# Optimization experiments

Hardware: AMD Instinct MI355X
Metric: run time of the kernel (lower is better)

Reference implementation:

```python
import jax, jax.numpy as jnp
import numpy as np

K = 4096
D = 128
B = 8
T = 3000
EMA_DECAY = 0.99
EMA_EPS = 1e-05
DEAD_THRESHOLD = 2.0


def setup_inputs() -> dict:
    key = jax.random.key(0)
    k1, k2, k3 = jax.random.split(key, 3)
    z = jax.random.normal(k1, (B, D, T), dtype=jnp.float32)
    codebook = jax.random.normal(k2, (K, D), dtype=jnp.float32) * 0.05  # pretrained-like
    ema_cluster_size = jnp.ones((K,), dtype=jnp.float32)
    ema_embed_avg = codebook.copy()
    return {"z": z, "codebook": codebook,
            "ema_cluster_size": ema_cluster_size, "ema_embed_avg": ema_embed_avg}


def reference(z, codebook, ema_cluster_size, ema_embed_avg):
    b, d, t = z.shape
    z_t = jnp.transpose(z, (0, 2, 1))            # [B, T, D]
    z_flat = z_t.reshape(-1, d)                  # [N, D]

    x2 = jnp.sum(z_flat * z_flat, axis=1, keepdims=True)
    y2 = jnp.sum(codebook * codebook, axis=1)[None, :]
    distances = x2 + y2 - 2.0 * (z_flat @ codebook.T)
    indices = jnp.argmin(distances, axis=1)      # [N]

    q = codebook[indices].reshape(b, t, d)       # [B, T, D]
    loss_commit = jnp.mean((z_t - jax.lax.stop_gradient(q)) ** 2)

    # --- EMA update (torch: @torch.no_grad, training mode) ---
    zf = jax.lax.stop_gradient(z_flat)
    counts = jax.ops.segment_sum(jnp.ones_like(indices, dtype=jnp.float32), indices, num_segments=K)
    embed_sum = jax.ops.segment_sum(zf, indices, num_segments=K)   # [K, D]
    new_cs = ema_cluster_size * EMA_DECAY + counts * (1.0 - EMA_DECAY)
    new_ea = ema_embed_avg * EMA_DECAY + embed_sum * (1.0 - EMA_DECAY)
    n = jnp.sum(new_cs)
    cluster_size = (new_cs + EMA_EPS) / (n + K * EMA_EPS) * n
    embed = new_ea / jnp.clip(cluster_size, 1e-12)[:, None]

    # dead-code reset: resample dead entries from the batch
    dead = new_cs < DEAD_THRESHOLD                                 # [K] bool
    rand_idx = jax.random.randint(jax.random.key(42), (K,), 0, zf.shape[0])
    sampled = zf[rand_idx]                                          # [K, D]
    new_codebook = jnp.where(dead[:, None], sampled, embed)
    new_cs = jnp.where(dead, 1.0, new_cs)
    new_ea = jnp.where(dead[:, None], sampled, new_ea)

    # straight-through estimator
    q_ste = z_t + jax.lax.stop_gradient(q - z_t)
    z_q = jnp.transpose(q_ste, (0, 2, 1))        # [B, D, T]
    codes = indices.reshape(b, t)[None, :, None, :]  # [1, B, 1, T]

    return (z_q, codes, loss_commit, new_codebook, new_cs, new_ea)
```

## Files before the change

kernel.cpp:

```cpp
#include <hip/hip_runtime.h>
#include <stdint.h>

#define KCB 4096
#define DIM 128
#define BSZ 8
#define TLEN 3000
#define NPT 24000
#define KD (KCB*DIM)
#define BDT (BSZ*DIM*TLEN)

#define OFF_ZQ    0
#define OFF_CODES 3072000
#define OFF_LOSS  3096000
#define OFF_CB    3096001
#define OFF_CS    3620289
#define OFF_EA    3624385

#define OUT_ZH    0
#define OUT_ZL    1536000
#define OUT_CBH   3096004
#define OUT_CBL   3358148

#define WS_LOSS   0
#define WS_NTOT   1
#define WS_RCNT   2
#define WS_COUNTS 16
#define WS_Y2     (WS_COUNTS + 4096)
#define WS_X2     (WS_Y2 + 4096)
#define WS_CS0    (WS_X2 + 24000)
#define WS_RAND   (WS_CS0 + 4096)
#define WS_IDX    (WS_RAND + 4096)
#define WS_RLIST  (WS_IDX + 24000)
#define RCAP      8192

#define EPS_CAND 2e-3f
#define CAND_MAX 8

#define NB_CB  16
#define NB_Z   375
#define NB_EA  2048
#define NB_ZQ  375

typedef __attribute__((ext_vector_type(8))) short bf16x8;
typedef __attribute__((ext_vector_type(4))) float f32x4;
typedef __attribute__((ext_vector_type(4))) int i32x4;

__device__ __forceinline__ unsigned short f2bf(float f) {
  uint32_t u = __float_as_uint(f);
  uint32_t r = (u + 0x7FFFu + ((u >> 16) & 1u)) >> 16;
  return (unsigned short)r;
}
__device__ __forceinline__ float bf2f(unsigned short h) {
  return __uint_as_float(((uint32_t)h) << 16);
}

__device__ __forceinline__ void async16(const void* g, void* l) {
  __builtin_amdgcn_global_load_lds(
      (const __attribute__((address_space(1))) void*)g,
      (__attribute__((address_space(3))) void*)l, 16, 0, 0);
}

__device__ __forceinline__ void threefry2x32(uint32_t k0, uint32_t k1,
                                             uint32_t x0, uint32_t x1,
                                             uint32_t& o0, uint32_t& o1) {
  const uint32_t ks0 = k0, ks1 = k1, ks2 = k0 ^ k1 ^ 0x1BD11BDAu;
  const int r0[4] = {13, 15, 26, 6};
  const int r1[4] = {17, 29, 16, 24};
  x0 += ks0; x1 += ks1;
  #pragma unroll
  for (int i = 0; i < 5; ++i) {
    #pragma unroll
    for (int j = 0; j < 4; ++j) {
      int r = (i & 1) ? r1[j] : r0[j];
      x0 += x1;
      x1 = (x1 << r) | (x1 >> (32 - r));
      x1 ^= x0;
    }
    uint32_t ia = (uint32_t)((i + 1) % 3), ib = (uint32_t)((i + 2) % 3);
    uint32_t a = (ia == 0) ? ks0 : (ia == 1) ? ks1 : ks2;
    uint32_t b = (ib == 0) ? ks0 : (ib == 1) ? ks1 : ks2;
    x0 += a;
    x1 += b + (uint32_t)(i + 1);
  }
  o0 = x0; o1 = x1;
}

__device__ __forceinline__ float np_sumsq_128(const float* __restrict__ v) {
  float r[8];
  #pragma unroll
  for (int j = 0; j < 8; ++j) r[j] = __fmul_rn(v[j], v[j]);
  #pragma unroll
  for (int i = 8; i < DIM; i += 8) {
    #pragma unroll
    for (int j = 0; j < 8; ++j)
      r[j] = __fadd_rn(r[j], __fmul_rn(v[i + j], v[i + j]));
  }
  return __fadd_rn(__fadd_rn(__fadd_rn(r[0], r[1]), __fadd_rn(r[2], r[3])),
                   __fadd_rn(__fadd_rn(r[4], r[5]), __fadd_rn(r[6], r[7])));
}

__global__ void prep_all_kernel(const float* __restrict__ z, const float* __restrict__ cb,
                                unsigned short* __restrict__ zh, unsigned short* __restrict__ zl,
                                float* __restrict__ x2,
                                unsigned short* __restrict__ cbh, unsigned short* __restrict__ cbl,
                                float* __restrict__ y2,
                                const float* __restrict__ ema_ea, float* __restrict__ out_ea) {
  __shared__ float zt[64 * 132];
  const int bid = blockIdx.x;
  const int tid = threadIdx.x;

  if (bid < NB_CB) {
    int k = bid * 256 + tid;
    const float4* row4 = (const float4*)(cb + (size_t)k * DIM);
    float racc[8];
    #pragma unroll
    for (int j = 0; j < 8; ++j) racc[j] = 0.f;
    #pragma unroll 4
    for (int c2 = 0; c2 < 16; ++c2) {
      float4 a = row4[c2 * 2], b = row4[c2 * 2 + 1];
      float f[8] = {a.x, a.y, a.z, a.w, b.x, b.y, b.z, b.w};
      i32x4 wh, wl;
      #pragma unroll
      for (int q = 0; q < 4; ++q) {
        float f0 = f[q * 2], f1 = f[q * 2 + 1];
        unsigned short h0 = f2bf(f0), h1 = f2bf(f1);
        unsigned short l0 = f2bf(f0 - bf2f(h0)), l1 = f2bf(f1 - bf2f(h1));
        wh[q] = (int)((uint32_t)h0 | ((uint32_t)h1 << 16));
        wl[q] = (int)((uint32_t)l0 | ((uint32_t)l1 << 16));
      }
      int cs = c2 ^ (k & 7);
      *(i32x4*)(cbh + (size_t)k * DIM + cs * 8) = wh;
      *(i32x4*)(cbl + (size_t)k * DIM + cs * 8) = wl;
      #pragma unroll
      for (int j = 0; j < 8; ++j)
        racc[j] = __fadd_rn(racc[j], __fmul_rn(f[j], f[j]));
    }
    y2[k] = __fadd_rn(__fadd_rn(__fadd_rn(racc[0], racc[1]), __fadd_rn(racc[2], racc[3])),
                      __fadd_rn(__fadd_rn(racc[4], racc[5]), __fadd_rn(racc[6], racc[7])));
  } else if (bid < NB_CB + NB_Z) {
    const int n0 = (bid - NB_CB) * 64;
    {
      int nl = tid & 63, dd = tid >> 6;
      int n = n0 + nl;
      int b = n / TLEN, t = n - b * TLEN;
      const float* zbase = z + (size_t)b * (DIM * TLEN) + t;
      #pragma unroll
      for (int d = dd; d < DIM; d += 4) zt[nl * 132 + d] = zbase[(size_t)d * TLEN];
    }
    __syncthreads();
    if (tid < 64) x2[n0 + tid] = np_sumsq_128(zt + tid * 132);

    int r = tid >> 2, d0 = (tid & 3) * 32;
    const float* src = zt + r * 132 + d0;
    size_t base = (size_t)(n0 + r) * 128 + d0;
    #pragma unroll
    for (int c = 0; c < 4; ++c) {
      i32x4 wh, wl;
      #pragma unroll
      for (int q = 0; q < 4; ++q) {
        float f0 = -2.0f * src[c * 8 + q * 2], f1 = -2.0f * src[c * 8 + q * 2 + 1];
        unsigned short h0 = f2bf(f0), h1 = f2bf(f1);
        unsigned short l0 = f2bf(f0 - bf2f(h0)), l1 = f2bf(f1 - bf2f(h1));
        wh[q] = (int)((uint32_t)h0 | ((uint32_t)h1 << 16));
        wl[q] = (int)((uint32_t)l0 | ((uint32_t)l1 << 16));
      }
      *(i32x4*)(zh + base + c * 8) = wh;
      *(i32x4*)(zl + base + c * 8) = wl;
    }
  } else {
    int i = (bid - NB_CB - NB_Z) * 256 + tid;
    out_ea[i] = 0.99f * ema_ea[i];
  }
}

__launch_bounds__(256)
__global__ void mfma_argmin_kernel(const unsigned short* __restrict__ zh,
                                   const unsigned short* __restrict__ zl,
                                   const unsigned short* __restrict__ cbh,
                                   const unsigned short* __restrict__ cbl,
                                   const float* __restrict__ y2g,
                                   const float* __restrict__ x2g,
                                   const float* __restrict__ z,
                                   const float* __restrict__ cb,
                                   int* __restrict__ idx_out,
                                   float* __restrict__ codes_out,
                                   int* __restrict__ rcnt,
                                   int* __restrict__ rlist) {
  __shared__ alignas(16) unsigned short zh_t[64 * 128];
  __shared__ alignas(16) unsigned short zl_t[64 * 128];
  __shared__ alignas(16) unsigned short Ah_t[64 * 128];
  __shared__ alignas(16) unsigned short Al_t[64 * 128];
  __shared__ float tv[64 * 24];
  __shared__ int   ti[64 * 24];

  const int tid = threadIdx.x;
  const int wv = tid >> 6, lane = tid & 63;
  const int kw = wv & 1, nw = wv >> 1;
  const int lg = lane >> 4, lc = lane & 15;
  const int n0 = blockIdx.x * 64;

  {
    const char* gh = (const char*)cbh + (size_t)(wv * 4) * 1024 + lane * 16;
    const char* gl_ = (const char*)cbl + (size_t)(wv * 4) * 1024 + lane * 16;
    char* lh = (char*)Ah_t + wv * 4096;
    char* ll = (char*)Al_t + wv * 4096;
    #pragma unroll
    for (int i = 0; i < 4; ++i) {
      async16(gh + i * 1024, lh + i * 1024);
      async16(gl_ + i * 1024, ll + i * 1024);
    }
  }

  {
    int r = tid >> 2, c0 = (tid & 3) * 4;
    const i32x4* gzh = (const i32x4*)(zh + (size_t)(n0 + r) * 128);
    const i32x4* gzl = (const i32x4*)(zl + (size_t)(n0 + r) * 128);
    #pragma unroll
    for (int c = 0; c < 4; ++c) {
      int cc = (c0 + c) ^ (r & 7);
      ((i32x4*)zh_t)[r * 16 + cc] = gzh[c0 + c];
      ((i32x4*)zl_t)[r * 16 + cc] = gzl[c0 + c];
    }
  }

  float t1v[2], t2v[2], t3v[2];
  int   t1i[2], t2i[2], t3i[2];
  #pragma unroll
  for (int ns = 0; ns < 2; ++ns) {
    t1v[ns] = t2v[ns] = t3v[ns] = 3.402823466e+38f;
    t1i[ns] = t2i[ns] = t3i[ns] = 0x7FFFFFFF;
  }

  const int arow0 = kw * 32 + lc,  arow1 = kw * 32 + 16 + lc;
  const int zrow0 = nw * 32 + lc,  zrow1 = nw * 32 + 16 + lc;

  for (int tile = 0; tile < 64; ++tile) {
    asm volatile("s_waitcnt vmcnt(0)" ::: "memory");
    __syncthreads();

    const int kb = tile * 64 + kw * 32;
    float4 y40 = *(const float4*)(y2g + kb + lg * 4);
    float4 y41 = *(const float4*)(y2g + kb + 16 + lg * 4);
    f32x4 acc[2][2];
    #pragma unroll
    for (int ns = 0; ns < 2; ++ns) {
      acc[0][ns][0] = y40.x; acc[0][ns][1] = y40.y; acc[0][ns][2] = y40.z; acc[0][ns][3] = y40.w;
      acc[1][ns][0] = y41.x; acc[1][ns][1] = y41.y; acc[1][ns][2] = y41.z; acc[1][ns][3] = y41.w;
    }

    #pragma unroll
    for (int ds = 0; ds < 4; ++ds) {
      int cA0 = (ds * 4 + lg) ^ (arow0 & 7);
      int cA1 = (ds * 4 + lg) ^ (arow1 & 7);
      bf16x8 a0h = *(const bf16x8*)&Ah_t[arow0 * 128 + cA0 * 8];
      bf16x8 a0l = *(const bf16x8*)&Al_t[arow0 * 128 + cA0 * 8];
      bf16x8 a1h = *(const bf16x8*)&Ah_t[arow1 * 128 + cA1 * 8];
      bf16x8 a1l = *(const bf16x8*)&Al_t[arow1 * 128 + cA1 * 8];
      int cz0 = (ds * 4 + lg) ^ (zrow0 & 7);
      int cz1 = (ds * 4 + lg) ^ (zrow1 & 7);
      bf16x8 z0h = *(const bf16x8*)&zh_t[zrow0 * 128 + cz0 * 8];
      bf16x8 z0l = *(const bf16x8*)&zl_t[zrow0 * 128 + cz0 * 8];
      bf16x8 z1h = *(const bf16x8*)&zh_t[zrow1 * 128 + cz1 * 8];
      bf16x8 z1l = *(const bf16x8*)&zl_t[zrow1 * 128 + cz1 * 8];
      acc[0][0] = __builtin_amdgcn_mfma_f32_16x16x32_bf16(a0h, z0h, acc[0][0], 0, 0, 0);
      acc[0][0] = __builtin_amdgcn_mfma_f32_16x16x32_bf16(a0h, z0l, acc[0][0], 0, 0, 0);
      acc[0][0] = __builtin_amdgcn_mfma_f32_16x16x32_bf16(a0l, z0h, acc[0][0], 0, 0, 0);
      acc[0][1] = __builtin_amdgcn_mfma_f32_16x16x32_bf16(a0h, z1h, acc[0][1], 0, 0, 0);
      acc[0][1] = __builtin_amdgcn_mfma_f32_16x16x32_bf16(a0h, z1l, acc[0][1], 0, 0, 0);
      acc[0][1] = __builtin_amdgcn_mfma_f32_16x16x32_bf16(a0l, z1h, acc[0][1], 0, 0, 0);
      acc[1][0] = __builtin_amdgcn_mfma_f32_16x16x32_bf16(a1h, z0h, acc[1][0], 0, 0, 0);
      acc[1][0] = __builtin_amdgcn_mfma_f32_16x16x32_bf16(a1h, z0l, acc[1][0], 0, 0, 0);
      acc[1][0] = __builtin_amdgcn_mfma_f32_16x16x32_bf16(a1l, z0h, acc[1][0], 0, 0, 0);
      acc[1][1] = __builtin_amdgcn_mfma_f32_16x16x32_bf16(a1h, z1h, acc[1][1], 0, 0, 0);
      acc[1][1] = __builtin_amdgcn_mfma_f32_16x16x32_bf16(a1h, z1l, acc[1][1], 0, 0, 0);
      acc[1][1] = __builtin_amdgcn_mfma_f32_16x16x32_bf16(a1l, z1h, acc[1][1], 0, 0, 0);
    }

    __syncthreads();

    if (tile + 1 < 64) {
      const char* gh = (const char*)cbh + (size_t)(tile + 1) * 16384 + (size_t)(wv * 4) * 1024 + lane * 16;
      const char* gl_ = (const char*)cbl + (size_t)(tile + 1) * 16384 + (size_t)(wv * 4) * 1024 + lane * 16;
      char* lh = (char*)Ah_t + wv * 4096;
      char* ll = (char*)Al_t + wv * 4096;
      #pragma unroll
      for (int i = 0; i < 4; ++i) {
        async16(gh + i * 1024, lh + i * 1024);
        async16(gl_ + i * 1024, ll + i * 1024);
      }
    }

    #pragma unroll
    for (int ks = 0; ks < 2; ++ks) {
      int kbase = kb + ks * 16 + lg * 4;
      #pragma unroll
      for (int ns = 0; ns < 2; ++ns) {
        float fm = fminf(fminf(acc[ks][ns][0], acc[ks][ns][1]),
                         fminf(acc[ks][ns][2], acc[ks][ns][3]));
        if (fm < t3v[ns]) {
          #pragma unroll
          for (int q = 0; q < 4; ++q) {
            float v = acc[ks][ns][q];
            int kidx = kbase + q;
            bool c1 = v < t1v[ns], c2 = v < t2v[ns], c3 = v < t3v[ns];
            float n3v = c2 ? t2v[ns] : (c3 ? v : t3v[ns]);
            int   n3i = c2 ? t2i[ns] : (c3 ? kidx : t3i[ns]);
            float n2v = c1 ? t1v[ns] : (c2 ? v : t2v[ns]);
            int   n2i = c1 ? t1i[ns] : (c2 ? kidx : t2i[ns]);
            t1v[ns] = c1 ? v : t1v[ns]; t1i[ns] = c1 ? kidx : t1i[ns];
            t2v[ns] = n2v; t2i[ns] = n2i;
            t3v[ns] = n3v; t3i[ns] = n3i;
          }
        }
      }
    }
  }

  #pragma unroll
  for (int ns = 0; ns < 2; ++ns) {
    int row = nw * 32 + ns * 16 + lc;
    int base = row * 24 + (kw * 4 + lg) * 3;
    tv[base + 0] = t1v[ns]; ti[base + 0] = t1i[ns];
    tv[base + 1] = t2v[ns]; ti[base + 1] = t2i[ns];
    tv[base + 2] = t3v[ns]; ti[base + 2] = t3i[ns];
  }
  __syncthreads();

  if (tid < 64) {
    int n = n0 + tid;
    float bv = 3.402823466e+38f; int bi = 0x7FFFFFFF;
    for (int e = 0; e < 24; ++e) {
      float v = tv[tid * 24 + e]; int i2 = ti[tid * 24 + e];
      if (v < bv || (v == bv && i2 < bi)) { bv = v; bi = i2; }
    }
    int ci[CAND_MAX]; int cnt = 0;
    float lim = bv + EPS_CAND;
    for (int e = 0; e < 24; ++e) {
      float v = tv[tid * 24 + e];
      if (v <= lim && cnt < CAND_MAX) {
        int x = ti[tid * 24 + e];
        int p = cnt++;
        while (p > 0 && ci[p - 1] > x) { ci[p] = ci[p - 1]; --p; }
        ci[p] = x;
      }
    }
    if (cnt == 1) {
      idx_out[n] = ci[0];
      codes_out[n] = (float)ci[0];
    } else {
      int slot = atomicAdd(rcnt, 1);
      if (slot < RCAP) {
        int* e = rlist + slot * 10;
        e[0] = n; e[1] = cnt;
        for (int c = 0; c < CAND_MAX; ++c) e[2 + c] = (c < cnt) ? ci[c] : 0;
        idx_out[n] = ci[0];
        codes_out[n] = (float)ci[0];
      } else {
        int b = n / TLEN, t = n - b * TLEN;
        const float* zr = z + (size_t)b * (DIM * TLEN) + t;
        float bestv = 0.f; int kbest = ci[0];
        for (int c = 0; c < cnt; ++c) {
          int k = ci[c];
          const float* cr = cb + (size_t)k * DIM;
          float dot = 0.f;
          for (int d = 0; d < DIM; ++d)
            dot = __fmaf_rn(zr[(size_t)d * TLEN], cr[d], dot);
          float tt = __fadd_rn(x2g[n], y2g[k]);
          float dist = __fsub_rn(tt, __fmul_rn(2.0f, dot));
          if (c == 0 || dist < bestv) { bestv = dist; kbest = k; }
        }
        idx_out[n] = kbest;
        codes_out[n] = (float)kbest;
      }
    }
  }
}

__global__ void rescore_kernel(const float* __restrict__ z, const float* __restrict__ cb,
                               const float* __restrict__ x2g, const float* __restrict__ y2g,
                               const int* __restrict__ rcnt, const int* __restrict__ rlist,
                               int* __restrict__ idx_out, float* __restrict__ codes_out) {
  int w = (blockIdx.x * 256 + threadIdx.x) >> 6;
  int lane = threadIdx.x & 63;
  int nw = (gridDim.x * 256) >> 6;
  int total = *rcnt; if (total > RCAP) total = RCAP;
  for (int i = w; i < total; i += nw) {
    const int* e = rlist + i * 10;
    int n = e[0], cnt = e[1];
    int b = n / TLEN, t = n - b * TLEN;
    const float* zr = z + (size_t)b * (DIM * TLEN) + t;
    float dist = 3.402823466e+38f;
    int k = e[2 + (lane < cnt ? lane : 0)];
    if (lane < cnt) {
      const float* cr = cb + (size_t)k * DIM;
      float dot = 0.f;
      #pragma unroll 8
      for (int d = 0; d < DIM; ++d)
        dot = __fmaf_rn(zr[(size_t)d * TLEN], cr[d], dot);
      float tt = __fadd_rn(x2g[n], y2g[k]);
      dist = __fsub_rn(tt, __fmul_rn(2.0f, dot));
    }
    float bestv = 0.f; int kbest = 0;
    for (int c = 0; c < cnt; ++c) {
      float v = __shfl(dist, c);
      int kk = __shfl(k, c);
      if (c == 0 || v < bestv) { bestv = v; kbest = kk; }
    }
    if (lane == 0) {
      idx_out[n] = kbest;
      codes_out[n] = (float)kbest;
    }
  }
}

__global__ void ea_scatter_kernel(const unsigned short* __restrict__ zh,
                                  const unsigned short* __restrict__ zl,
                                  const int* __restrict__ idx,
                                  float* __restrict__ ea_out,
                                  float* __restrict__ counts) {
  int n = (blockIdx.x * 256 + threadIdx.x) >> 6;
  int lane = threadIdx.x & 63;
  int k = idx[n];
  uint32_t h = *(const uint32_t*)(zh + (size_t)n * 128 + lane * 2);
  uint32_t l = *(const uint32_t*)(zl + (size_t)n * 128 + lane * 2);
  float f0 = bf2f((unsigned short)(h & 0xffffu)) + bf2f((unsigned short)(l & 0xffffu));
  float f1 = bf2f((unsigned short)(h >> 16)) + bf2f((unsigned short)(l >> 16));
  float* dst = ea_out + (size_t)k * DIM + lane * 2;
  atomicAdd(dst, -0.005f * f0);
  atomicAdd(dst + 1, -0.005f * f1);
  if (lane == 0) atomicAdd(counts + k, 1.0f);
}

__global__ void zq_cs_kernel(const float* __restrict__ z, const float* __restrict__ cb,
                             const int* __restrict__ idx,
                             float* __restrict__ zq_out, float* __restrict__ loss_ws,
                             const float* __restrict__ ema_cs, const float* __restrict__ counts,
                             float* __restrict__ cs0, uint32_t* __restrict__ rnd,
                             float* __restrict__ ntot) {
  __shared__ float qt[64 * 132];
  __shared__ float ps[4];
  const int bid = blockIdx.x;
  const int tid = threadIdx.x;

  if (bid < NB_ZQ) {
    const int n0 = bid * 64;
    {
      int r = tid >> 2, c = tid & 3;
      int k = idx[n0 + r];
      const float4* src = (const float4*)(cb + (size_t)k * DIM) + c * 8;
      float4* dst = (float4*)(qt + r * 132) + c * 8;
      #pragma unroll
      for (int j = 0; j < 8; ++j) dst[j] = src[j];
    }
    __syncthreads();
    int nl = tid & 63, dd = tid >> 6;
    int n = n0 + nl;
    int b = n / TLEN, t = n - b * TLEN;
    float* zqb = zq_out + (size_t)b * (DIM * TLEN) + t;
    const float* zb = z + (size_t)b * (DIM * TLEN) + t;
    float sq = 0.f;
    #pragma unroll
    for (int d = dd; d < DIM; d += 4) {
      float q = qt[nl * 132 + d];
      zqb[(size_t)d * TLEN] = q;
      float diff = zb[(size_t)d * TLEN] - q;
      sq = fmaf(diff, diff, sq);
    }
    #pragma unroll
    for (int m = 1; m <= 32; m <<= 1) sq += __shfl_xor(sq, m);
    if ((tid & 63) == 0) ps[tid >> 6] = sq;
    __syncthreads();
    if (tid == 0) atomicAdd(loss_ws, ps[0] + ps[1] + ps[2] + ps[3]);
  } else {
    int k = (bid - NB_ZQ) * 256 + tid;
    float v = 0.99f * ema_cs[k] + 0.01f * counts[k];
    cs0[k] = v;

    uint32_t o0, o1;
    threefry2x32(0u, 42u, 0u, (uint32_t)k, o0, o1);
    uint32_t bits = o0 ^ o1;
    uint32_t hi = bits >> 16, lo = bits & 0xffffu;
    const uint32_t span = 24000u, mult = 23296u;
    uint32_t off = ((hi % span) * mult + (lo % span)) % span;
    rnd[k] = off;

    float s = v;
    #pragma unroll
    for (int m = 1; m <= 32; m <<= 1) s += __shfl_xor(s, m);
    if ((tid & 63) == 0) ps[tid >> 6] = s;
    __syncthreads();
    if (tid == 0) atomicAdd(ntot, ps[0] + ps[1] + ps[2] + ps[3]);
  }
}

__global__ void finalize_kernel(const float* __restrict__ z, const float* __restrict__ cs0_ws,
                                const uint32_t* __restrict__ rnd,
                                const float* __restrict__ ntot_ws, const float* __restrict__ loss_ws,
                                float* __restrict__ out) {
  int i = blockIdx.x * 256 + threadIdx.x;
  int k = i >> 7, d = i & (DIM - 1);
  float cs0 = cs0_ws[k];
  float ntot = *ntot_ws;
  float* ea = out + OFF_EA;
  float ea0 = ea[i];
  float csz = (cs0 + 1e-5f) / (ntot + (float)KCB * 1e-5f) * ntot;
  float embed = ea0 / fmaxf(csz, 1e-12f);
  bool dead = cs0 < 2.0f;
  uint32_t rn = rnd[k];
  int bb = (int)(rn / TLEN), tt = (int)(rn % TLEN);
  float sampled = z[(size_t)bb * (DIM * TLEN) + (size_t)d * TLEN + tt];
  out[OFF_CB + i] = dead ? sampled : embed;
  ea[i] = dead ? sampled : ea0;
  if (d == 0) out[OFF_CS + k] = dead ? 1.0f : cs0;
  if (i == 0) out[OFF_LOSS] = (*loss_ws) * (1.0f / (float)BDT);
}

extern "C" void kernel_launch(void* const* d_in, const int* in_sizes, int n_in,
                              void* d_out, int out_size, void* d_ws, size_t ws_size,
                              hipStream_t stream) {
  const float* z      = (const float*)d_in[0];
  const float* cb     = (const float*)d_in[1];
  const float* ema_cs = (const float*)d_in[2];
  const float* ema_ea = (const float*)d_in[3];
  float* out = (float*)d_out;
  float* wsf = (float*)d_ws;

  unsigned short* zh  = (unsigned short*)(out + OUT_ZH);
  unsigned short* zl  = (unsigned short*)(out + OUT_ZL);
  unsigned short* cbh = (unsigned short*)(out + OUT_CBH);
  unsigned short* cbl = (unsigned short*)(out + OUT_CBL);

  hipMemsetAsync(d_ws, 0, (size_t)(16 + 4096) * sizeof(float), stream);

  prep_all_kernel<<<NB_CB + NB_Z + NB_EA, 256, 0, stream>>>(
      z, cb, zh, zl, wsf + WS_X2, cbh, cbl, wsf + WS_Y2, ema_ea, out + OFF_EA);

  mfma_argmin_kernel<<<NPT / 64, 256, 0, stream>>>(zh, zl, cbh, cbl,
                                                   wsf + WS_Y2, wsf + WS_X2,
                                                   z, cb,
                                                   (int*)(wsf + WS_IDX), out + OFF_CODES,
                                                   (int*)(wsf + WS_RCNT), (int*)(wsf + WS_RLIST));
  rescore_kernel<<<64, 256, 0, stream>>>(z, cb, wsf + WS_X2, wsf + WS_Y2,
                                         (const int*)(wsf + WS_RCNT), (const int*)(wsf + WS_RLIST),
                                         (int*)(wsf + WS_IDX), out + OFF_CODES);

  ea_scatter_kernel<<<NPT * 64 / 256, 256, 0, stream>>>(zh, zl, (int*)(wsf + WS_IDX),
                                                        out + OFF_EA, wsf + WS_COUNTS);
  zq_cs_kernel<<<NB_ZQ + 16, 256, 0, stream>>>(z, cb, (int*)(wsf + WS_IDX),
                                               out + OFF_ZQ, wsf + WS_LOSS,
                                               ema_cs, wsf + WS_COUNTS,
                                               wsf + WS_CS0, (uint32_t*)(wsf + WS_RAND),
                                               wsf + WS_NTOT);
  finalize_kernel<<<KD / 256, 256, 0, stream>>>(z, wsf + WS_CS0, (uint32_t*)(wsf + WS_RAND),
                                                wsf + WS_NTOT, wsf + WS_LOSS, out);
}
```

Before: 224.6 us.

## Fuse EMA embed-sum scatter into argmin and rescore kernels

Removes the separate ea_scatter kernel. The argmin kernel now scatters each resolved row's z values, read from its existing shared-memory tile, into ea_out along with its count. Rows sent to rescoring are scattered by the rescore kernel once the final index is known. This saves a kernel launch and a global re-read of zh/zl and idx. In exchange the argmin kernel gains an extra barrier and an atomic-heavy tail, and each thread issues 32 serial atomics, which may lengthen that kernel.

```diff
diff --git a/kernel.cpp b/kernel.cpp
--- a/kernel.cpp
+++ b/kernel.cpp
@@ -185,13 +185,16 @@
                                    int* __restrict__ idx_out,
                                    float* __restrict__ codes_out,
                                    int* __restrict__ rcnt,
-                                   int* __restrict__ rlist) {
+                                   int* __restrict__ rlist,
+                                   float* __restrict__ ea_out,
+                                   float* __restrict__ counts) {
   __shared__ alignas(16) unsigned short zh_t[64 * 128];
   __shared__ alignas(16) unsigned short zl_t[64 * 128];
   __shared__ alignas(16) unsigned short Ah_t[64 * 128];
   __shared__ alignas(16) unsigned short Al_t[64 * 128];
   __shared__ float tv[64 * 24];
   __shared__ int   ti[64 * 24];
+  __shared__ int   rowk[64];
 
   const int tid = threadIdx.x;
   const int wv = tid >> 6, lane = tid & 63;
@@ -347,6 +350,7 @@
     if (cnt == 1) {
       idx_out[n] = ci[0];
       codes_out[n] = (float)ci[0];
+      rowk[tid] = ci[0];
     } else {
       int slot = atomicAdd(rcnt, 1);
       if (slot < RCAP) {
@@ -355,6 +359,7 @@
         for (int c = 0; c < CAND_MAX; ++c) e[2 + c] = (c < cnt) ? ci[c] : 0;
         idx_out[n] = ci[0];
         codes_out[n] = (float)ci[0];
+        rowk[tid] = -1;
       } else {
         int b = n / TLEN, t = n - b * TLEN;
         const float* zr = z + (size_t)b * (DIM * TLEN) + t;
@@ -371,7 +376,26 @@
         }
         idx_out[n] = kbest;
         codes_out[n] = (float)kbest;
-      }
+        rowk[tid] = kbest;
+      }
+    }
+  }
+  __syncthreads();
+
+  {
+    int r = tid >> 2;
+    int k = rowk[r];
+    if (k >= 0) {
+      int dbase = (tid & 3) * 32;
+      float* dst = ea_out + (size_t)k * DIM;
+      #pragma unroll 8
+      for (int j = 0; j < 32; ++j) {
+        int d = dbase + j;
+        int idxs = r * 128 + (((d >> 3) ^ (r & 7)) << 3) + (d & 7);
+        float v = bf2f(zh_t[idxs]) + bf2f(zl_t[idxs]);
+        atomicAdd(dst + d, -0.005f * v);
+      }
+      if ((tid & 3) == 0) atomicAdd(counts + k, 1.0f);
     }
   }
 }
@@ -379,7 +403,10 @@
 __global__ void rescore_kernel(const float* __restrict__ z, const float* __restrict__ cb,
                                const float* __restrict__ x2g, const float* __restrict__ y2g,
                                const int* __restrict__ rcnt, const int* __restrict__ rlist,
-                               int* __restrict__ idx_out, float* __restrict__ codes_out) {
+                               const unsigned short* __restrict__ zh,
+                               const unsigned short* __restrict__ zl,
+                               int* __restrict__ idx_out, float* __restrict__ codes_out,
+                               float* __restrict__ ea_out, float* __restrict__ counts) {
   int w = (blockIdx.x * 256 + threadIdx.x) >> 6;
   int lane = threadIdx.x & 63;
   int nw = (gridDim.x * 256) >> 6;
@@ -406,29 +433,21 @@
       int kk = __shfl(k, c);
       if (c == 0 || v < bestv) { bestv = v; kbest = kk; }
     }
+    {
+      const unsigned short* zhr = zh + (size_t)n * 128 + lane * 2;
+      const unsigned short* zlr = zl + (size_t)n * 128 + lane * 2;
+      float v0 = bf2f(zhr[0]) + bf2f(zlr[0]);
+      float v1 = bf2f(zhr[1]) + bf2f(zlr[1]);
+      float* dst = ea_out + (size_t)kbest * DIM + lane * 2;
+      atomicAdd(dst, -0.005f * v0);
+      atomicAdd(dst + 1, -0.005f * v1);
+    }
     if (lane == 0) {
+      atomicAdd(counts + kbest, 1.0f);
       idx_out[n] = kbest;
       codes_out[n] = (float)kbest;
     }
   }
-}
-
-__global__ void ea_scatter_kernel(const unsigned short* __restrict__ zh,
-                                  const unsigned short* __restrict__ zl,
-                                  const int* __restrict__ idx,
-                                  float* __restrict__ ea_out,
-                                  float* __restrict__ counts) {
-  int n = (blockIdx.x * 256 + threadIdx.x) >> 6;
-  int lane = threadIdx.x & 63;
-  int k = idx[n];
-  uint32_t h = *(const uint32_t*)(zh + (size_t)n * 128 + lane * 2);
-  uint32_t l = *(const uint32_t*)(zl + (size_t)n * 128 + lane * 2);
-  float f0 = bf2f((unsigned short)(h & 0xffffu)) + bf2f((unsigned short)(l & 0xffffu));
-  float f1 = bf2f((unsigned short)(h >> 16)) + bf2f((unsigned short)(l >> 16));
-  float* dst = ea_out + (size_t)k * DIM + lane * 2;
-  atomicAdd(dst, -0.005f * f0);
-  atomicAdd(dst + 1, -0.005f * f1);
-  if (lane == 0) atomicAdd(counts + k, 1.0f);
 }
 
 __global__ void zq_cs_kernel(const float* __restrict__ z, const float* __restrict__ cb,
@@ -539,13 +558,13 @@
                                                    wsf + WS_Y2, wsf + WS_X2,
                                                    z, cb,
                                                    (int*)(wsf + WS_IDX), out + OFF_CODES,
-                                                   (int*)(wsf + WS_RCNT), (int*)(wsf + WS_RLIST));
+                                                   (int*)(wsf + WS_RCNT), (int*)(wsf + WS_RLIST),
+                                                   out + OFF_EA, wsf + WS_COUNTS);
   rescore_kernel<<<64, 256, 0, stream>>>(z, cb, wsf + WS_X2, wsf + WS_Y2,
                                          (const int*)(wsf + WS_RCNT), (const int*)(wsf + WS_RLIST),
-                                         (int*)(wsf + WS_IDX), out + OFF_CODES);
-
-  ea_scatter_kernel<<<NPT * 64 / 256, 256, 0, stream>>>(zh, zl, (int*)(wsf + WS_IDX),
-                                                        out + OFF_EA, wsf + WS_COUNTS);
+                                         zh, zl,
+                                         (int*)(wsf + WS_IDX), out + OFF_CODES,
+                                         out + OFF_EA, wsf + WS_COUNTS);
   zq_cs_kernel<<<NB_ZQ + 16, 256, 0, stream>>>(z, cb, (int*)(wsf + WS_IDX),
                                                out + OFF_ZQ, wsf + WS_LOSS,
                                                ema_cs, wsf + WS_COUNTS,
```

Result: slower. 356.8 us (+58.8%).
